# Kernel optimization log

Hardware: AMD Instinct MI355X
Metric: run time of the kernel (lower is better)

The kernel has to match this reference:

```python
import jax, jax.numpy as jnp
import numpy as np


def setup_inputs() -> dict:
    key = jax.random.key(0)
    k1, k2 = jax.random.split(key)
    x = jax.random.normal(k1, (4, 4096, 1024), dtype=jnp.float32)
    codebook = jax.random.normal(k2, (16384, 1024), dtype=jnp.float32)
    return {"x": x, "codebook": codebook}


def reference(x, codebook):
    # Euclidean snap: argmin over pairwise L2 distances, then gather.
    # Squared distances suffice for argmin (monotone transform of cdist p=2).
    x2 = jnp.sum(x * x, axis=-1, keepdims=True)            # [b, n, 1]
    c2 = jnp.sum(codebook * codebook, axis=-1)             # [c]
    xc = jnp.einsum('bnd,cd->bnc', x, codebook)            # [b, n, c]
    d2 = x2 - 2.0 * xc + c2                                # [b, n, c]
    codebook_ids = jnp.argmin(d2, axis=-1)                 # [b, n]
    output = jnp.take(codebook, codebook_ids, axis=0)      # [b, n, d]
    return output
```

## Files before the change

### kernel.cpp

```cpp
#include <hip/hip_runtime.h>
#include <hip/hip_bf16.h>
#include <hip/hip_fp8.h>
#include <stdint.h>

#define NROWS  16384
#define NCODES 16384
#define DIM    1024
#define NT     16
#define MARGIN_Q 514

typedef float f32x4  __attribute__((ext_vector_type(4)));
typedef short bf16x8 __attribute__((ext_vector_type(8)));
typedef unsigned char uchar;

__device__ __forceinline__ ushort f2bf(float f) {
  uint32_t u = __float_as_uint(f);
  uint32_t r = u + 0x7FFFu + ((u >> 16) & 1u);
  return (ushort)(r >> 16);
}
__device__ __forceinline__ int imin(int a, int b){ return a < b ? a : b; }
__device__ __forceinline__ int imax(int a, int b){ return a < b ? b : a; }
__device__ __forceinline__ int packKey32(float s, int idx) {
  int q = (int)rintf(s * 16.0f);
  return q * 16384 + idx;
}

#define GLDS16(gp, lp) \
  __builtin_amdgcn_global_load_lds((const __attribute__((address_space(1))) void*)(gp), \
                                   (__attribute__((address_space(3))) void*)(lp), 16, 0, 0)

__device__ __forceinline__ void sbar() {
  asm volatile("" ::: "memory");
  __builtin_amdgcn_s_barrier();
  asm volatile("" ::: "memory");
}

__global__ __launch_bounds__(256) void c2_kernel(const float* __restrict__ cb,
                                                 float* __restrict__ c2) {
  const int code = blockIdx.x;
  const int t = threadIdx.x, lane = t & 63, wid = t >> 6;
  f32x4 v = *(const f32x4*)(cb + (size_t)code * DIM + t * 4);
  float s = v[0]*v[0] + v[1]*v[1] + v[2]*v[2] + v[3]*v[3];
  #pragma unroll
  for (int off = 32; off; off >>= 1) s += __shfl_down(s, off);
  __shared__ float part[4];
  if (lane == 0) part[wid] = s;
  __syncthreads();
  if (t == 0) c2[code] = part[0] + part[1] + part[2] + part[3];
}

__global__ __launch_bounds__(256) void convert_fp8_swz(const float* __restrict__ src,
                                                       uchar* __restrict__ dst) {
  const int chunk = blockIdx.x * 256 + threadIdx.x;
  const int p   = chunk & 3;
  const int row = (chunk >> 2) & 255;
  const int kt  = (chunk >> 10) & 15;
  const int m   = chunk >> 14;
  const int c   = p ^ ((row & 7) >> 1);
  const float* s = src + (size_t)(m * 256 + row) * DIM + kt * 64 + c * 16;
  uchar b[16];
  #pragma unroll
  for (int j = 0; j < 16; ++j) {
    __hip_fp8_e4m3 h(s[j]);
    b[j] = h.__x;
  }
  uint64_t lo = 0, hi = 0;
  #pragma unroll
  for (int j = 0; j < 8; ++j) { lo |= (uint64_t)b[j] << (8 * j); hi |= (uint64_t)b[j + 8] << (8 * j); }
  uint64_t* o = (uint64_t*)(dst + (size_t)chunk * 16);
  if (row & 1) { o[0] = hi; o[1] = lo; }
  else         { o[0] = lo; o[1] = hi; }
}


#define STAGE_A(BUF, KT) do {                                                     \
    GLDS16(ga + (KT)*16384,        &lsA[BUF][w*1024]);                            \
    GLDS16(ga + (KT)*16384 + 8192, &lsA[BUF][w*1024 + 8192]);                     \
  } while (0)
#define STAGE_B(BUF, KT) do {                                                     \
    GLDS16(gb + (KT)*16384,        &lsB[BUF][w*1024]);                            \
    GLDS16(gb + (KT)*16384 + 8192, &lsB[BUF][w*1024 + 8192]);                     \
  } while (0)

#define RD_A(MIB, BUF) do {                                                       \
    _Pragma("unroll")                                                             \
    for (int mi_ = 0; mi_ < 4; ++mi_) {                                           \
      aF[mi_][0] = *(const long*)(A0[BUF] + ((MIB) + mi_) * 1024);                \
      aF[mi_][1] = *(const long*)(A1[BUF] + ((MIB) + mi_) * 1024);                \
    } } while (0)
#define RD_Bx(DST, NIB, BUF) do {                                                 \
    _Pragma("unroll")                                                             \
    for (int ni_ = 0; ni_ < 2; ++ni_) {                                           \
      DST[ni_][0] = *(const long*)(B0[BUF] + ((NIB) + ni_) * 1024);               \
      DST[ni_][1] = *(const long*)(B1[BUF] + ((NIB) + ni_) * 1024);               \
    } } while (0)

#define MMA_Q(MB, NB, AF, BF) do {                                                \
    __builtin_amdgcn_s_setprio(1);                                                \
    _Pragma("unroll")                                                             \
    for (int ks_ = 0; ks_ < 2; ++ks_) {                                           \
      _Pragma("unroll")                                                           \
      for (int mi_ = 0; mi_ < 4; ++mi_) {                                         \
        _Pragma("unroll")                                                         \
        for (int ni_ = 0; ni_ < 2; ++ni_)                                         \
          acc[(MB) + mi_][(NB) + ni_] = __builtin_amdgcn_mfma_f32_16x16x32_fp8_fp8( \
              AF[mi_][ks_], BF[ni_][ks_], acc[(MB) + mi_][(NB) + ni_], 0, 0, 0);  \
      } }                                                                         \
    __builtin_amdgcn_s_setprio(0);                                                \
  } while (0)

#define G4  asm volatile("s_waitcnt vmcnt(4)" ::: "memory")
#define G0  asm volatile("s_waitcnt vmcnt(0)" ::: "memory")
#define NOG do {} while (0)

#define TILE(KT, AC, BC, AN, BN_, DOST, GUARD) do {                               \
    RD_Bx(bF0, 0, BC);                                                            \
    RD_Bx(bF1, 2, BC);                                                            \
    asm volatile("s_waitcnt lgkmcnt(0)" ::: "memory");                            \
    sbar();                                                        \
    if (DOST) { STAGE_A(AN, (KT) + 2); STAGE_B(BN_, (KT) + 2); }                  \
    RD_A(0, AC);                                                                  \
    MMA_Q(0, 0, aF, bF0);                                                         \
    MMA_Q(0, 2, aF, bF1);                                                         \
    RD_A(4, AC);                                                                  \
    MMA_Q(4, 0, aF, bF0);                                                         \
    MMA_Q(4, 2, aF, bF1);                                                         \
    asm volatile("s_waitcnt lgkmcnt(0)" ::: "memory");                            \
    GUARD;                                                                        \
    sbar();                                                        \
  } while (0)

__global__ __launch_bounds__(512, 2) void snap_gemm256(const uchar* __restrict__ xs,
                                                       const uchar* __restrict__ cs,
                                                       const float* __restrict__ c2,
                                                       int* __restrict__ cand) {
  __shared__ uchar lsA[3][16384];
  __shared__ uchar lsB[2][16384];

  const int t    = threadIdx.x;
  const int lane = t & 63;
  const int w    = t >> 6;
  const int wm   = w >> 2;
  const int wn   = w & 3;
  const int l15  = lane & 15;
  const int kgrp = lane >> 4;

  const int bid = blockIdx.x;
  const int swz = (bid & 7) * 512 + (bid >> 3);
  const int bm  = swz & 63;
  const int bn  = swz >> 6;

  const uchar* ga = xs + (size_t)bm * 16 * 16384 + w * 1024 + lane * 16;
  const uchar* gb = cs + (size_t)bn * 16 * 16384 + w * 1024 + lane * 16;

  const int sw0  = (( kgrp)      ^ (l15 & 7)) * 8;
  const int sw1  = ((4 | kgrp)   ^ (l15 & 7)) * 8;
  const int arow = (wm * 128 + l15) * 64;
  const int brow = (wn * 64  + l15) * 64;
  const uchar* A0[3]; const uchar* A1[3];
  const uchar* B0[2]; const uchar* B1[2];
  #pragma unroll
  for (int b = 0; b < 3; ++b) { A0[b] = &lsA[b][arow + sw0]; A1[b] = &lsA[b][arow + sw1]; }
  #pragma unroll
  for (int b = 0; b < 2; ++b) { B0[b] = &lsB[b][brow + sw0]; B1[b] = &lsB[b][brow + sw1]; }

  f32x4 acc[8][4];
  #pragma unroll
  for (int mi = 0; mi < 8; ++mi)
    #pragma unroll
    for (int ni = 0; ni < 4; ++ni)
      acc[mi][ni] = (f32x4){0.f, 0.f, 0.f, 0.f};

  long aF[4][2], bF0[2][2], bF1[2][2];

  STAGE_A(0, 0); STAGE_B(0, 0);
  STAGE_A(1, 1); STAGE_B(1, 1);
  G4;
  sbar();

  TILE(0 , 0, 0, 2, 0, 1, G4);
  TILE(1 , 1, 1, 0, 1, 1, G4);
  TILE(2 , 2, 0, 1, 0, 1, G4);
  TILE(3 , 0, 1, 2, 1, 1, G4);
  TILE(4 , 1, 0, 0, 0, 1, G4);
  TILE(5 , 2, 1, 1, 1, 1, G4);
  TILE(6 , 0, 0, 2, 0, 1, G4);
  TILE(7 , 1, 1, 0, 1, 1, G4);
  TILE(8 , 2, 0, 1, 0, 1, G4);
  TILE(9 , 0, 1, 2, 1, 1, G4);
  TILE(10, 1, 0, 0, 0, 1, G4);
  TILE(11, 2, 1, 1, 1, 1, G4);
  TILE(12, 0, 0, 2, 0, 1, G4);
  TILE(13, 1, 1, 0, 1, 1, G4);
  TILE(14, 2, 0, 1, 0, 0, G0);
  TILE(15, 0, 1, 2, 1, 0, NOG);

  __syncthreads();

  int* red = (int*)&lsA[0][0];
  float c2v[4];
  int   colv[4];
  #pragma unroll
  for (int ni = 0; ni < 4; ++ni) {
    colv[ni] = bn * 256 + wn * 64 + ni * 16 + l15;
    c2v[ni]  = c2[colv[ni]];
  }

  #pragma unroll
  for (int mi = 0; mi < 8; ++mi) {
    #pragma unroll
    for (int r = 0; r < 4; ++r) {
      int a = packKey32(fmaf(-2.0f, acc[mi][0][r], c2v[0]), colv[0]);
      int b = packKey32(fmaf(-2.0f, acc[mi][1][r], c2v[1]), colv[1]);
      int c = packKey32(fmaf(-2.0f, acc[mi][2][r], c2v[2]), colv[2]);
      int d = packKey32(fmaf(-2.0f, acc[mi][3][r], c2v[3]), colv[3]);
      int lo1 = imin(a, b), hi1 = imax(a, b);
      int lo2 = imin(c, d), hi2 = imax(c, d);
      int k1 = imin(lo1, lo2);
      int k2 = imin(imax(lo1, lo2), imin(hi1, hi2));
      #pragma unroll
      for (int m = 1; m < 16; m <<= 1) {
        int o1 = __shfl_xor(k1, m);
        int o2 = __shfl_xor(k2, m);
        int n1 = imin(k1, o1);
        int n2 = imin(imax(k1, o1), imin(k2, o2));
        k1 = n1; k2 = n2;
      }
      if (l15 == 0) {
        int rl = wm * 128 + mi * 16 + kgrp * 4 + r;
        red[(wn * 256 + rl) * 2 + 0] = k1;
        red[(wn * 256 + rl) * 2 + 1] = k2;
      }
    }
  }
  __syncthreads();

  if (t < 256) {
    int k1 = red[(0 * 256 + t) * 2 + 0];
    int k2 = red[(0 * 256 + t) * 2 + 1];
    #pragma unroll
    for (int q = 1; q < 4; ++q) {
      int p1 = red[(q * 256 + t) * 2 + 0];
      int p2 = red[(q * 256 + t) * 2 + 1];
      int n1 = imin(k1, p1);
      int n2 = imin(imax(k1, p1), imin(k2, p2));
      k1 = n1; k2 = n2;
    }
    size_t o = (size_t)(bm * 256 + t) * 128 + (size_t)bn * 2;
    cand[o]     = k1;
    cand[o + 1] = k2;
  }
}

__global__ __launch_bounds__(256) void snap_gemm_slow(const float* __restrict__ x,
                                                      const float* __restrict__ cb,
                                                      const float* __restrict__ c2,
                                                      int* __restrict__ cand) {
  __shared__ ushort lsA[2][8192];
  __shared__ ushort lsB[2][8192];
  __shared__ int redbuf[2][128][2];

  const int t    = threadIdx.x;
  const int lane = t & 63;
  const int wid  = t >> 6;
  const int wm   = wid & 1;
  const int wn   = wid >> 1;
  const int l15  = lane & 15;
  const int kgrp = lane >> 4;

  const int bm = blockIdx.x & 127;
  const int bn = blockIdx.x >> 7;
  const int rowBase = bm * 128;
  const int colBase = bn * 128;

  const float* aptr[4];
  const float* bptr[4];
  int ldsOff[4];
  #pragma unroll
  for (int i = 0; i < 4; ++i) {
    int pc = t + 256 * i;
    int row = pc >> 3;
    int g = (pc & 7) ^ (row & 7);
    aptr[i] = x  + (size_t)(rowBase + row) * DIM + g * 8;
    bptr[i] = cb + (size_t)(colBase + row) * DIM + g * 8;
    ldsOff[i] = pc * 8;
  }

  f32x4 acc[4][4];
  #pragma unroll
  for (int mi = 0; mi < 4; ++mi)
    #pragma unroll
    for (int ni = 0; ni < 4; ++ni)
      acc[mi][ni] = (f32x4){0.f, 0.f, 0.f, 0.f};

  auto STAGE = [&](int buf, int kt) {
    const int kOff = kt * 64;
    #pragma unroll
    for (int i = 0; i < 4; ++i) {
      f32x4 a0 = *(const f32x4*)(aptr[i] + kOff);
      f32x4 a1 = *(const f32x4*)(aptr[i] + kOff + 4);
      f32x4 b0 = *(const f32x4*)(bptr[i] + kOff);
      f32x4 b1 = *(const f32x4*)(bptr[i] + kOff + 4);
      bf16x8 pa, pb;
      #pragma unroll
      for (int j = 0; j < 4; ++j) {
        pa[j]     = (short)f2bf(a0[j]);
        pa[j + 4] = (short)f2bf(a1[j]);
        pb[j]     = (short)f2bf(b0[j]);
        pb[j + 4] = (short)f2bf(b1[j]);
      }
      *(bf16x8*)(&lsA[buf][ldsOff[i]]) = pa;
      *(bf16x8*)(&lsB[buf][ldsOff[i]]) = pb;
    }
  };

  STAGE(0, 0);
  __syncthreads();

  for (int kt = 0; kt < DIM / 64; ++kt) {
    const int cur = kt & 1;
    if (kt < DIM / 64 - 1) STAGE(cur ^ 1, kt + 1);

    const ushort* bA = &lsA[cur][0];
    const ushort* bB = &lsB[cur][0];
    #pragma unroll
    for (int ks = 0; ks < 2; ++ks) {
      const int gidx = ks * 4 + kgrp;
      bf16x8 af[4], bfr[4];
      #pragma unroll
      for (int mi = 0; mi < 4; ++mi) {
        int r_ = wm * 64 + mi * 16 + l15;
        af[mi] = *(const bf16x8*)(bA + (r_ * 8 + (gidx ^ (r_ & 7))) * 8);
      }
      #pragma unroll
      for (int ni = 0; ni < 4; ++ni) {
        int c_ = wn * 64 + ni * 16 + l15;
        bfr[ni] = *(const bf16x8*)(bB + (c_ * 8 + (gidx ^ (c_ & 7))) * 8);
      }
      #pragma unroll
      for (int mi = 0; mi < 4; ++mi)
        #pragma unroll
        for (int ni = 0; ni < 4; ++ni)
          acc[mi][ni] = __builtin_amdgcn_mfma_f32_16x16x32_bf16(af[mi], bfr[ni], acc[mi][ni], 0, 0, 0);
    }
    __syncthreads();
  }

  float c2v[4];
  int   colv[4];
  #pragma unroll
  for (int ni = 0; ni < 4; ++ni) {
    colv[ni] = colBase + wn * 64 + ni * 16 + l15;
    c2v[ni]  = c2[colv[ni]];
  }

  #pragma unroll
  for (int mi = 0; mi < 4; ++mi) {
    #pragma unroll
    for (int r = 0; r < 4; ++r) {
      int a = packKey32(fmaf(-2.0f, acc[mi][0][r], c2v[0]), colv[0]);
      int b = packKey32(fmaf(-2.0f, acc[mi][1][r], c2v[1]), colv[1]);
      int c = packKey32(fmaf(-2.0f, acc[mi][2][r], c2v[2]), colv[2]);
      int d = packKey32(fmaf(-2.0f, acc[mi][3][r], c2v[3]), colv[3]);
      int lo1 = imin(a, b), hi1 = imax(a, b);
      int lo2 = imin(c, d), hi2 = imax(c, d);
      int k1 = imin(lo1, lo2);
      int k2 = imin(imax(lo1, lo2), imin(hi1, hi2));
      #pragma unroll
      for (int m = 1; m < 16; m <<= 1) {
        int o1 = __shfl_xor(k1, m);
        int o2 = __shfl_xor(k2, m);
        int n1 = imin(k1, o1);
        int n2 = imin(imax(k1, o1), imin(k2, o2));
        k1 = n1; k2 = n2;
      }
      if (l15 == 0) {
        int rl = wm * 64 + mi * 16 + kgrp * 4 + r;
        redbuf[wn][rl][0] = k1;
        redbuf[wn][rl][1] = k2;
      }
    }
  }
  __syncthreads();

  if (t < 128) {
    int a1 = redbuf[0][t][0], a2 = redbuf[0][t][1];
    int b1 = redbuf[1][t][0], b2 = redbuf[1][t][1];
    int m1 = imin(a1, b1);
    int m2 = imin(imax(a1, b1), imin(a2, b2));
    size_t o = (size_t)(rowBase + t) * 256 + (size_t)bn * 2;
    cand[o]     = m1;
    cand[o + 1] = m2;
  }
}

__global__ __launch_bounds__(256) void rerank(const float* __restrict__ x,
                                              const float* __restrict__ cb,
                                              const int* __restrict__ cand,
                                              int* __restrict__ bestidx,
                                              int poolN) {
  const int row = blockIdx.x;
  const int t = threadIdx.x, lane = t & 63, wid = t >> 6;
  __shared__ int    smin[4];
  __shared__ int    gshared;
  __shared__ double dpart[4];
  __shared__ int    cnt;
  __shared__ int    list[64];

  int my = (t < poolN) ? cand[(size_t)row * poolN + t] : 0x7FFFFFFF;
  int k = my;
  #pragma unroll
  for (int off = 32; off; off >>= 1) k = imin(k, __shfl_down(k, off));
  if (lane == 0) smin[wid] = k;
  if (t == 0) cnt = 0;
  __syncthreads();
  if (t == 0) {
    int g = smin[0];
    for (int i = 1; i < 4; ++i) g = imin(g, smin[i]);
    gshared = g;
  }
  __syncthreads();

  const int gq = gshared >> 14;
  if ((my >> 14) <= gq + MARGIN_Q) {
    int p = atomicAdd(&cnt, 1);
    if (p < 64) list[p] = my & 16383;
  }
  __syncthreads();
  int n = cnt; if (n > 64) n = 64;

  uint64_t best = ~0ull;
  const float* xr = x + (size_t)row * DIM;
  for (int i = 0; i < n; ++i) {
    const int cidx = list[i];
    const float* cr = cb + (size_t)cidx * DIM;
    double p = 0.0;
    #pragma unroll
    for (int j = 0; j < 4; ++j) {
      int d = t + 256 * j;
      double diff = (double)xr[d] - (double)cr[d];
      p += diff * diff;
    }
    #pragma unroll
    for (int off = 32; off; off >>= 1) p += __shfl_down(p, off);
    if (lane == 0) dpart[wid] = p;
    __syncthreads();
    if (t == 0) {
      double d2 = dpart[0] + dpart[1] + dpart[2] + dpart[3];
      uint64_t bits = (uint64_t)__double_as_longlong(d2);
      uint64_t key = (bits & ~0x3FFFull) | (uint32_t)cidx;
      if (key < best) best = key;
    }
    __syncthreads();
  }
  if (t == 0) bestidx[row] = (int)(best & 0x3FFFull);
}

__global__ __launch_bounds__(256) void gather_rows(const float* __restrict__ cb,
                                                   const int* __restrict__ bestidx,
                                                   float* __restrict__ out) {
  const int row = blockIdx.x;
  const int idx = bestidx[row];
  f32x4 v = *(const f32x4*)(cb + (size_t)idx * DIM + threadIdx.x * 4);
  *(f32x4*)(out + (size_t)row * DIM + threadIdx.x * 4) = v;
}

extern "C" void kernel_launch(void* const* d_in, const int* in_sizes, int n_in,
                              void* d_out, int out_size, void* d_ws, size_t ws_size,
                              hipStream_t stream) {
  const float* x  = (const float*)d_in[0];
  const float* cb = (const float*)d_in[1];
  float* out = (float*)d_out;

  float* c2      = (float*)d_ws;
  int*   bestidx = (int*)((char*)d_ws + 64 * 1024);

  const size_t candBytes = (size_t)NROWS * 128 * 4;
  const size_t needFast  = 128 * 1024 + candBytes;

  c2_kernel<<<NCODES, 256, 0, stream>>>(cb, c2);

  if (ws_size >= needFast) {
    uchar* xs = (uchar*)d_out;
    uchar* cs = xs + (size_t)NROWS * DIM;
    int* cand = (int*)((char*)d_ws + 128 * 1024);

    convert_fp8_swz<<<4096, 256, 0, stream>>>(x,  xs);
    convert_fp8_swz<<<4096, 256, 0, stream>>>(cb, cs);
    snap_gemm256<<<4096, 512, 0, stream>>>(xs, cs, c2, cand);
    rerank<<<NROWS, 256, 0, stream>>>(x, cb, cand, bestidx, 128);
    gather_rows<<<NROWS, 256, 0, stream>>>(cb, bestidx, out);
  } else {
    int* cand = (int*)d_out;
    snap_gemm_slow<<<(NROWS / 128) * (NCODES / 128), 256, 0, stream>>>(x, cb, c2, cand);
    rerank<<<NROWS, 256, 0, stream>>>(x, cb, cand, bestidx, 256);
    gather_rows<<<NROWS, 256, 0, stream>>>(cb, bestidx, out);
  }
}
```

Baseline: 645.2 us.

## Pair K-slices in fp8 layout for 16-byte LDS reads and double-buffer pipeline

The fp8 conversion now packs each lane's two MFMA k-slices (offsets j and j+32) next to each other in a 16-byte chunk, with a new XOR swizzle. The GEMM can then fetch both operand fragments with one 128-bit LDS read instead of two 64-bit reads. The LDS pipeline drops from a triple-buffered A with prefetch distance 2 to a plain double buffer with prefetch distance 1, a full vmcnt(0) wait, and a single barrier per tile. All B fragments are now loaded at once. This cuts LDS instruction count and LDS footprint, possibly raising occupancy, but it exposes more global-load latency at each tile.

```diff
diff --git a/kernel.cpp b/kernel.cpp
--- a/kernel.cpp
+++ b/kernel.cpp
@@ -11,6 +11,7 @@
 
 typedef float f32x4  __attribute__((ext_vector_type(4)));
 typedef short bf16x8 __attribute__((ext_vector_type(8)));
+typedef long  longx2 __attribute__((ext_vector_type(2)));
 typedef unsigned char uchar;
 
 __device__ __forceinline__ ushort f2bf(float f) {
@@ -49,27 +50,25 @@
   if (t == 0) c2[code] = part[0] + part[1] + part[2] + part[3];
 }
 
-__global__ __launch_bounds__(256) void convert_fp8_swz(const float* __restrict__ src,
-                                                       uchar* __restrict__ dst) {
+__global__ __launch_bounds__(256) void convert_fp8_pair(const float* __restrict__ src,
+                                                        uchar* __restrict__ dst) {
   const int chunk = blockIdx.x * 256 + threadIdx.x;
   const int p   = chunk & 3;
   const int row = (chunk >> 2) & 255;
   const int kt  = (chunk >> 10) & 15;
   const int m   = chunk >> 14;
-  const int c   = p ^ ((row & 7) >> 1);
-  const float* s = src + (size_t)(m * 256 + row) * DIM + kt * 64 + c * 16;
-  uchar b[16];
-  #pragma unroll
-  for (int j = 0; j < 16; ++j) {
-    __hip_fp8_e4m3 h(s[j]);
-    b[j] = h.__x;
-  }
+  const int q   = p ^ ((row >> 1) & 3);
+  const float* s = src + (size_t)(m * 256 + row) * DIM + kt * 64 + q * 8;
   uint64_t lo = 0, hi = 0;
   #pragma unroll
-  for (int j = 0; j < 8; ++j) { lo |= (uint64_t)b[j] << (8 * j); hi |= (uint64_t)b[j + 8] << (8 * j); }
+  for (int j = 0; j < 8; ++j) {
+    __hip_fp8_e4m3 a(s[j]);
+    __hip_fp8_e4m3 b(s[j + 32]);
+    lo |= (uint64_t)a.__x << (8 * j);
+    hi |= (uint64_t)b.__x << (8 * j);
+  }
   uint64_t* o = (uint64_t*)(dst + (size_t)chunk * 16);
-  if (row & 1) { o[0] = hi; o[1] = lo; }
-  else         { o[0] = lo; o[1] = hi; }
+  o[0] = lo; o[1] = hi;
 }
 
 
@@ -85,17 +84,17 @@
 #define RD_A(MIB, BUF) do {                                                       \
     _Pragma("unroll")                                                             \
     for (int mi_ = 0; mi_ < 4; ++mi_) {                                           \
-      aF[mi_][0] = *(const long*)(A0[BUF] + ((MIB) + mi_) * 1024);                \
-      aF[mi_][1] = *(const long*)(A1[BUF] + ((MIB) + mi_) * 1024);                \
+      longx2 v_ = *(const longx2*)(Apos[BUF] + ((MIB) + mi_) * 1024);             \
+      aF[mi_][0] = v_[0]; aF[mi_][1] = v_[1];                                     \
     } } while (0)
-#define RD_Bx(DST, NIB, BUF) do {                                                 \
+#define RD_B(BUF) do {                                                            \
     _Pragma("unroll")                                                             \
-    for (int ni_ = 0; ni_ < 2; ++ni_) {                                           \
-      DST[ni_][0] = *(const long*)(B0[BUF] + ((NIB) + ni_) * 1024);               \
-      DST[ni_][1] = *(const long*)(B1[BUF] + ((NIB) + ni_) * 1024);               \
+    for (int ni_ = 0; ni_ < 4; ++ni_) {                                           \
+      longx2 v_ = *(const longx2*)(Bpos[BUF] + ni_ * 1024);                       \
+      bF[ni_][0] = v_[0]; bF[ni_][1] = v_[1];                                     \
     } } while (0)
 
-#define MMA_Q(MB, NB, AF, BF) do {                                                \
+#define MMA_Q(MB, NB) do {                                                        \
     __builtin_amdgcn_s_setprio(1);                                                \
     _Pragma("unroll")                                                             \
     for (int ks_ = 0; ks_ < 2; ++ks_) {                                           \
@@ -104,37 +103,31 @@
         _Pragma("unroll")                                                         \
         for (int ni_ = 0; ni_ < 2; ++ni_)                                         \
           acc[(MB) + mi_][(NB) + ni_] = __builtin_amdgcn_mfma_f32_16x16x32_fp8_fp8( \
-              AF[mi_][ks_], BF[ni_][ks_], acc[(MB) + mi_][(NB) + ni_], 0, 0, 0);  \
+              aF[mi_][ks_], bF[(NB) + ni_][ks_], acc[(MB) + mi_][(NB) + ni_], 0, 0, 0); \
       } }                                                                         \
     __builtin_amdgcn_s_setprio(0);                                                \
   } while (0)
 
-#define G4  asm volatile("s_waitcnt vmcnt(4)" ::: "memory")
 #define G0  asm volatile("s_waitcnt vmcnt(0)" ::: "memory")
 #define NOG do {} while (0)
 
-#define TILE(KT, AC, BC, AN, BN_, DOST, GUARD) do {                               \
-    RD_Bx(bF0, 0, BC);                                                            \
-    RD_Bx(bF1, 2, BC);                                                            \
-    asm volatile("s_waitcnt lgkmcnt(0)" ::: "memory");                            \
-    sbar();                                                        \
-    if (DOST) { STAGE_A(AN, (KT) + 2); STAGE_B(BN_, (KT) + 2); }                  \
-    RD_A(0, AC);                                                                  \
-    MMA_Q(0, 0, aF, bF0);                                                         \
-    MMA_Q(0, 2, aF, bF1);                                                         \
-    RD_A(4, AC);                                                                  \
-    MMA_Q(4, 0, aF, bF0);                                                         \
-    MMA_Q(4, 2, aF, bF1);                                                         \
+#define TILE(KT, CUR, NXT, DOST, GUARD) do {                                      \
+    if (DOST) { STAGE_A(NXT, (KT) + 1); STAGE_B(NXT, (KT) + 1); }                 \
+    RD_B(CUR);                                                                    \
+    RD_A(0, CUR);                                                                 \
+    MMA_Q(0, 0); MMA_Q(0, 2);                                                     \
+    RD_A(4, CUR);                                                                 \
+    MMA_Q(4, 0); MMA_Q(4, 2);                                                     \
     asm volatile("s_waitcnt lgkmcnt(0)" ::: "memory");                            \
     GUARD;                                                                        \
-    sbar();                                                        \
+    sbar();                                                                       \
   } while (0)
 
 __global__ __launch_bounds__(512, 2) void snap_gemm256(const uchar* __restrict__ xs,
                                                        const uchar* __restrict__ cs,
                                                        const float* __restrict__ c2,
                                                        int* __restrict__ cand) {
-  __shared__ uchar lsA[3][16384];
+  __shared__ uchar lsA[2][16384];
   __shared__ uchar lsB[2][16384];
 
   const int t    = threadIdx.x;
@@ -153,16 +146,12 @@
   const uchar* ga = xs + (size_t)bm * 16 * 16384 + w * 1024 + lane * 16;
   const uchar* gb = cs + (size_t)bn * 16 * 16384 + w * 1024 + lane * 16;
 
-  const int sw0  = (( kgrp)      ^ (l15 & 7)) * 8;
-  const int sw1  = ((4 | kgrp)   ^ (l15 & 7)) * 8;
-  const int arow = (wm * 128 + l15) * 64;
-  const int brow = (wn * 64  + l15) * 64;
-  const uchar* A0[3]; const uchar* A1[3];
-  const uchar* B0[2]; const uchar* B1[2];
-  #pragma unroll
-  for (int b = 0; b < 3; ++b) { A0[b] = &lsA[b][arow + sw0]; A1[b] = &lsA[b][arow + sw1]; }
-  #pragma unroll
-  for (int b = 0; b < 2; ++b) { B0[b] = &lsB[b][brow + sw0]; B1[b] = &lsB[b][brow + sw1]; }
+  const int posoff = (kgrp ^ ((l15 >> 1) & 3)) * 16;
+  const int arow   = (wm * 128 + l15) * 64;
+  const int brow   = (wn * 64  + l15) * 64;
+  const uchar* Apos[2]; const uchar* Bpos[2];
+  #pragma unroll
+  for (int b = 0; b < 2; ++b) { Apos[b] = &lsA[b][arow + posoff]; Bpos[b] = &lsB[b][brow + posoff]; }
 
   f32x4 acc[8][4];
   #pragma unroll
@@ -171,29 +160,28 @@
     for (int ni = 0; ni < 4; ++ni)
       acc[mi][ni] = (f32x4){0.f, 0.f, 0.f, 0.f};
 
-  long aF[4][2], bF0[2][2], bF1[2][2];
+  long aF[4][2], bF[4][2];
 
   STAGE_A(0, 0); STAGE_B(0, 0);
-  STAGE_A(1, 1); STAGE_B(1, 1);
-  G4;
+  G0;
   sbar();
 
-  TILE(0 , 0, 0, 2, 0, 1, G4);
-  TILE(1 , 1, 1, 0, 1, 1, G4);
-  TILE(2 , 2, 0, 1, 0, 1, G4);
-  TILE(3 , 0, 1, 2, 1, 1, G4);
-  TILE(4 , 1, 0, 0, 0, 1, G4);
-  TILE(5 , 2, 1, 1, 1, 1, G4);
-  TILE(6 , 0, 0, 2, 0, 1, G4);
-  TILE(7 , 1, 1, 0, 1, 1, G4);
-  TILE(8 , 2, 0, 1, 0, 1, G4);
-  TILE(9 , 0, 1, 2, 1, 1, G4);
-  TILE(10, 1, 0, 0, 0, 1, G4);
-  TILE(11, 2, 1, 1, 1, 1, G4);
-  TILE(12, 0, 0, 2, 0, 1, G4);
-  TILE(13, 1, 1, 0, 1, 1, G4);
-  TILE(14, 2, 0, 1, 0, 0, G0);
-  TILE(15, 0, 1, 2, 1, 0, NOG);
+  TILE(0 , 0, 1, 1, G0);
+  TILE(1 , 1, 0, 1, G0);
+  TILE(2 , 0, 1, 1, G0);
+  TILE(3 , 1, 0, 1, G0);
+  TILE(4 , 0, 1, 1, G0);
+  TILE(5 , 1, 0, 1, G0);
+  TILE(6 , 0, 1, 1, G0);
+  TILE(7 , 1, 0, 1, G0);
+  TILE(8 , 0, 1, 1, G0);
+  TILE(9 , 1, 0, 1, G0);
+  TILE(10, 0, 1, 1, G0);
+  TILE(11, 1, 0, 1, G0);
+  TILE(12, 0, 1, 1, G0);
+  TILE(13, 1, 0, 1, G0);
+  TILE(14, 0, 1, 1, G0);
+  TILE(15, 1, 0, 0, NOG);
 
   __syncthreads();
 
@@ -485,8 +473,8 @@
     uchar* cs = xs + (size_t)NROWS * DIM;
     int* cand = (int*)((char*)d_ws + 128 * 1024);
 
-    convert_fp8_swz<<<4096, 256, 0, stream>>>(x,  xs);
-    convert_fp8_swz<<<4096, 256, 0, stream>>>(cb, cs);
+    convert_fp8_pair<<<4096, 256, 0, stream>>>(x,  xs);
+    convert_fp8_pair<<<4096, 256, 0, stream>>>(cb, cs);
     snap_gemm256<<<4096, 512, 0, stream>>>(xs, cs, c2, cand);
     rerank<<<NROWS, 256, 0, stream>>>(x, cb, cand, bestidx, 128);
     gather_rows<<<NROWS, 256, 0, stream>>>(cb, bestidx, out);
```

After: 591.9 us. 1.09x faster.
